# Performance work log

Measured on AMD Instinct MI355X. Metric: run time of the kernel, lower is better.

The kernel has to match this reference:

```python
import jax, jax.numpy as jnp
import numpy as np
import math

DIM = 1024
SEQ = 4096
BATCH = 4
CHUNK = 64
LN_EPS = 1e-5


def setup_inputs() -> dict:
    key = jax.random.key(0)
    ks = jax.random.split(key, 16)
    d = DIM
    def lin(k):
        k1, k2 = jax.random.split(k)
        lim = 1.0 / math.sqrt(d)
        W = jax.random.uniform(k1, (d, d), jnp.float32, -lim, lim)
        b = jax.random.uniform(k2, (d,), jnp.float32, -lim, lim)
        return W, b
    Wk, bk = lin(ks[0])
    Wv, bv = lin(ks[1])
    Wq, bq = lin(ks[2])
    Wkm, bkm = lin(ks[3])
    Wqm, bqm = lin(ks[4])
    Wo, bo = lin(ks[5])
    return {
        "x": jax.random.normal(ks[6], (BATCH, SEQ, d), jnp.float32),
        "base_phases": jax.random.normal(ks[7], (SEQ, d), jnp.float32) * math.pi,
        "Wk": Wk, "bk": bk, "Wv": Wv, "bv": bv, "Wq": Wq, "bq": bq,
        "Wkm": Wkm, "bkm": bkm, "Wqm": Wqm, "bqm": bqm,
        "mod_scale": jnp.ones((1,), jnp.float32) * 0.1,
        "ln_g": jnp.ones((d,), jnp.float32),
        "ln_b": jnp.zeros((d,), jnp.float32),
        "Wo": Wo, "bo": bo,
    }


def reference(x, base_phases, Wk, bk, Wv, bv, Wq, bq, Wkm, bkm, Wqm, bqm,
              mod_scale, ln_g, ln_b, Wo, bo):
    B, S, D = x.shape
    key = x @ Wk + bk
    value = x @ Wv + bv
    query = x @ Wq + bq
    base = base_phases[:S][None]                      # [1,S,D]
    key_phase = base + (key @ Wkm + bkm) * mod_scale   # [B,S,D]
    query_phase = base + (query @ Wqm + bqm) * mod_scale
    bound_real = value * jnp.cos(key_phase)
    bound_imag = value * jnp.sin(key_phase)
    pad = (CHUNK - S % CHUNK) % CHUNK
    if pad > 0:
        pcfg = ((0, 0), (0, pad), (0, 0))
        bound_real = jnp.pad(bound_real, pcfg)
        bound_imag = jnp.pad(bound_imag, pcfg)
        query_phase = jnp.pad(query_phase, pcfg)
    P = S + pad
    nc = P // CHUNK
    br = bound_real.reshape(B, nc, CHUNK, D)
    bi = bound_imag.reshape(B, nc, CHUNK, D)
    qp = query_phase.reshape(B, nc, CHUNK, D)
    mem_real = jnp.cumsum(br, axis=2)
    mem_imag = jnp.cumsum(bi, axis=2)
    retrieved = mem_real * jnp.cos(qp) + mem_imag * jnp.sin(qp)
    retrieved = retrieved.reshape(B, P, D)[:, :S] / math.sqrt(D)
    mu = jnp.mean(retrieved, axis=-1, keepdims=True)
    var = jnp.mean(jnp.square(retrieved - mu), axis=-1, keepdims=True)
    normed = (retrieved - mu) * jax.lax.rsqrt(var + LN_EPS) * ln_g + ln_b
    out = normed @ Wo + bo
    return x + out
```

## Files before the change

### kernel.cpp

```cpp
#include <hip/hip_runtime.h>

#define DIM 1024
#define SEQ 4096
#define MROWS 16384
#define CHUNK 64
#define NCHUNKBLKS 256

typedef float  f32x4  __attribute__((ext_vector_type(4)));
typedef __bf16 bf16x8 __attribute__((ext_vector_type(8)));
typedef __bf16 bf16x4 __attribute__((ext_vector_type(4)));

__device__ __forceinline__ void gld16(const void* g, void* l) {
  __builtin_amdgcn_global_load_lds((__attribute__((address_space(1))) void*)g,
                                   (__attribute__((address_space(3))) void*)l,
                                   16, 0, 0);
}

__device__ __forceinline__ f32x4 ld4f(const __bf16* p) {
  bf16x4 v = *(const bf16x4*)p;
  f32x4 r;
#pragma unroll
  for (int j = 0; j < 4; ++j) r[j] = (float)v[j];
  return r;
}

#define KLOOP64(As_, Bs_, Ag_, Bg_, AsL_, BsL_)                                  \
  for (int kt = 0; kt < DIM / 64; ++kt) {                                        \
    const __bf16* a_ = Ag_ + kt * 64;                                            \
    const __bf16* b_ = Bg_ + kt * 64;                                            \
    _Pragma("unroll") for (int i = 0; i < 4; ++i) {                              \
      gld16(a_ + i * 32 * DIM, AsL_ + i * 4096);                                 \
      gld16(b_ + i * 32 * DIM, BsL_ + i * 4096);                                 \
    }                                                                            \
    __syncthreads();                                                             \
    const bf16x8* Av_ = (const bf16x8*)(As_);                                    \
    const bf16x8* Bv_ = (const bf16x8*)(Bs_);                                    \
    _Pragma("unroll") for (int kk = 0; kk < 2; ++kk) {                           \
      bf16x8 af[4], bfv[4];                                                      \
      const int pc = (kk * 4 + kg) ^ (lane & 7);                                 \
      _Pragma("unroll") for (int i = 0; i < 4; ++i) af[i]  = Av_[(ar + i*16)*8 + pc]; \
      _Pragma("unroll") for (int i = 0; i < 4; ++i) bfv[i] = Bv_[(br + i*16)*8 + pc]; \
      _Pragma("unroll") for (int mi = 0; mi < 4; ++mi)                           \
        _Pragma("unroll") for (int ni = 0; ni < 4; ++ni)                         \
          acc[mi][ni] = __builtin_amdgcn_mfma_f32_16x16x32_bf16(af[mi], bfv[ni], acc[mi][ni], 0, 0, 0); \
    }                                                                            \
    __syncthreads();                                                             \
  }

#define GEMM_PROLOG64(A_, B_)                                                    \
  const int tid  = threadIdx.x;                                                  \
  const int lane = tid & 63;                                                     \
  const int widx = tid >> 6;                                                     \
  const int wr   = widx >> 1, wc = widx & 1;                                     \
  const int kc = ((lane & 7) ^ ((lane >> 3) & 7)) * 8;                           \
  const __bf16* Ag = (A_) + (size_t)(row0 + widx * 8 + (lane >> 3)) * DIM + kc;  \
  const __bf16* Bg = (B_) + (size_t)(col0 + widx * 8 + (lane >> 3)) * DIM + kc;  \
  char* AsL = (char*)As + widx * 1024;                                           \
  char* BsL = (char*)Bs + widx * 1024;                                           \
  f32x4 acc[4][4] = {};                                                          \
  const int ar = wr * 64 + (lane & 15);                                          \
  const int br = wc * 64 + (lane & 15);                                          \
  const int kg = lane >> 4;

template <int MODE, int SWZ>
__global__ __launch_bounds__(256, 2)
void gemm_bt(const __bf16* __restrict__ A, const __bf16* __restrict__ Bt,
             const float* __restrict__ bias, void* __restrict__ outp,
             const float* __restrict__ mscp, const float* __restrict__ xres,
             const __bf16* __restrict__ A2, const __bf16* __restrict__ Bt2,
             void* __restrict__ out2)
{
  __shared__ __bf16 As[128 * 64];
  __shared__ __bf16 Bs[128 * 64];
  if (MODE == 5 && blockIdx.z == 1) { A = A2; Bt = Bt2; outp = out2; }

  int row_t, col_t;
  if (SWZ == 1) {
    const int b = blockIdx.y * 8 + blockIdx.x;
    const int xcd = b & 7, slot = b >> 3;
    col_t = slot & 7;
    row_t = (xcd << 4) | (slot >> 3);
  } else {
    row_t = blockIdx.y; col_t = blockIdx.x;
  }
  const int row0 = row_t * 128, col0 = col_t * 128;

  GEMM_PROLOG64(A, Bt)
  KLOOP64(As, Bs, Ag, Bg, AsL, BsL)

  const int ccol = col0 + wc * 64 + (lane & 15);
  const int crow = row0 + wr * 64 + kg * 4;
  float bvv[4];
  if (MODE != 5) {
#pragma unroll
    for (int ni = 0; ni < 4; ++ni) bvv[ni] = bias[ccol + ni * 16];
  }
  float ms = 0.f;
  if (MODE == 5) ms = mscp[0];
#pragma unroll
  for (int mi = 0; mi < 4; ++mi)
#pragma unroll
    for (int ni = 0; ni < 4; ++ni)
#pragma unroll
      for (int r = 0; r < 4; ++r) {
        const int row = crow + mi * 16 + r;
        const int col = ccol + ni * 16;
        const size_t idx = (size_t)row * DIM + col;
        if (MODE == 3) {
          ((float*)outp)[idx] = acc[mi][ni][r] + bvv[ni] + xres[idx];
        } else {
          ((__bf16*)outp)[idx] = (__bf16)(acc[mi][ni][r] * ms);
        }
      }
}

__global__ __launch_bounds__(256, 2)
void gemm3(const __bf16* __restrict__ A, const __bf16* __restrict__ Ball,
           const float* __restrict__ biasAll,
           __bf16* __restrict__ valb, __bf16* __restrict__ kphb,
           __bf16* __restrict__ qphb)
{
  __shared__ __bf16 As[128 * 64];
  __shared__ __bf16 Bs[128 * 64];
  const int b = blockIdx.y * 24 + blockIdx.x;
  const int xcd = b & 7, p = b >> 3;
  const int col_t = p / 16;
  const int row_t = (xcd << 4) + (p & 15);
  const int row0 = row_t * 128, col0 = col_t * 128;

  GEMM_PROLOG64(A, Ball)
  KLOOP64(As, Bs, Ag, Bg, AsL, BsL)

  const int band = col_t >> 3;
  const int ccol = col0 + wc * 64 + (lane & 15);
  const int lcol0 = ccol & 1023;
  const int crow = row0 + wr * 64 + kg * 4;
  float bvv[4];
#pragma unroll
  for (int ni = 0; ni < 4; ++ni) bvv[ni] = biasAll[ccol + ni * 16];
  __bf16* outb = (band == 0) ? valb : (band == 1) ? kphb : qphb;
#pragma unroll
  for (int mi = 0; mi < 4; ++mi)
#pragma unroll
    for (int ni = 0; ni < 4; ++ni)
#pragma unroll
      for (int r = 0; r < 4; ++r) {
        const int row = crow + mi * 16 + r;
        const size_t idx = (size_t)row * DIM + lcol0 + ni * 16;
        outb[idx] = (__bf16)(acc[mi][ni][r] + bvv[ni]);
      }
}

__global__ __launch_bounds__(256)
void phasor_ln(const __bf16* __restrict__ val, const __bf16* __restrict__ kph,
               const __bf16* __restrict__ qph, const __bf16* __restrict__ baseb,
               const float* __restrict__ g, const float* __restrict__ lb,
               __bf16* __restrict__ nb)
{
  const int t = threadIdx.x;
  const int w = t >> 6, lane = t & 63;
  const size_t r0 = (size_t)blockIdx.x * CHUNK;
  const int c = t * 4;
  const f32x4 gv  = ((const f32x4*)g)[t];
  const f32x4 lbv = ((const f32x4*)lb)[t];
  __shared__ float redS[8][4], redQ[8][4];
  float mr[4] = {0.f, 0.f, 0.f, 0.f};
  float mi[4] = {0.f, 0.f, 0.f, 0.f};
  for (int rb = 0; rb < 8; ++rb) {
    float ret[8][4], ss[8], qq[8];
#pragma unroll
    for (int r = 0; r < 8; ++r) {
      const int row = rb * 8 + r;
      const size_t base = (r0 + row) * DIM + c;
      const f32x4 v  = ld4f(val + base);
      const f32x4 kp = ld4f(kph + base);
      const f32x4 qp = ld4f(qph + base);
      const f32x4 bp = ld4f(baseb + (size_t)((r0 + row) & (SEQ - 1)) * DIM + c);
      float s = 0.f, q = 0.f;
#pragma unroll
      for (int j = 0; j < 4; ++j) {
        float sk, ck, sq, cq;
        __sincosf(bp[j] + kp[j], &sk, &ck);
        mr[j] += v[j] * ck;
        mi[j] += v[j] * sk;
        __sincosf(bp[j] + qp[j], &sq, &cq);
        ret[r][j] = (mr[j] * cq + mi[j] * sq) * 0.03125f;
        s += ret[r][j];
        q += ret[r][j] * ret[r][j];
      }
      ss[r] = s; qq[r] = q;
    }
#pragma unroll
    for (int off = 32; off > 0; off >>= 1)
#pragma unroll
      for (int r = 0; r < 8; ++r) {
        ss[r] += __shfl_down(ss[r], off);
        qq[r] += __shfl_down(qq[r], off);
      }
    if (lane == 0)
#pragma unroll
      for (int r = 0; r < 8; ++r) { redS[r][w] = ss[r]; redQ[r][w] = qq[r]; }
    __syncthreads();
#pragma unroll
    for (int r = 0; r < 8; ++r) {
      const float mu   = (redS[r][0] + redS[r][1] + redS[r][2] + redS[r][3]) * (1.0f / DIM);
      const float varr = (redQ[r][0] + redQ[r][1] + redQ[r][2] + redQ[r][3]) * (1.0f / DIM) - mu * mu;
      const float rinv = rsqrtf(varr + 1e-5f);
      bf16x4 o;
#pragma unroll
      for (int j = 0; j < 4; ++j) o[j] = (__bf16)((ret[r][j] - mu) * rinv * gv[j] + lbv[j]);
      *(bf16x4*)(nb + (r0 + rb * 8 + r) * DIM + c) = o;
    }
    __syncthreads();
  }
}

__global__ void f2b_kernel(const float* __restrict__ in, __bf16* __restrict__ out, int n4) {
  int i = blockIdx.x * 256 + threadIdx.x;
  if (i >= n4) return;
  f32x4 vv = ((const f32x4*)in)[i];
  bf16x4 o;
#pragma unroll
  for (int j = 0; j < 4; ++j) o[j] = (__bf16)vv[j];
  ((bf16x4*)out)[i] = o;
}

__global__ void wrapb_kernel(const float* __restrict__ in, __bf16* __restrict__ out, int n4) {
  int i = blockIdx.x * 256 + threadIdx.x;
  if (i >= n4) return;
  f32x4 vv = ((const f32x4*)in)[i];
  bf16x4 o;
#pragma unroll
  for (int j = 0; j < 4; ++j) {
    float v = vv[j];
    v -= 6.2831853f * rintf(v * 0.15915494f);
    o[j] = (__bf16)v;
  }
  ((bf16x4*)out)[i] = o;
}

__global__ void f2b2_kernel(const float* __restrict__ i0, __bf16* __restrict__ o0,
                            const float* __restrict__ i1, __bf16* __restrict__ o1, int n4) {
  int i = blockIdx.x * 256 + threadIdx.x;
  if (i >= n4) return;
  const float* in = blockIdx.y ? i1 : i0;
  __bf16* out = blockIdx.y ? o1 : o0;
  f32x4 vv = ((const f32x4*)in)[i];
  bf16x4 o;
#pragma unroll
  for (int j = 0; j < 4; ++j) o[j] = (__bf16)vv[j];
  ((bf16x4*)out)[i] = o;
}

__global__ void transpose_f2b4(const float* __restrict__ s0, __bf16* __restrict__ d0,
                               const float* __restrict__ s1, __bf16* __restrict__ d1,
                               const float* __restrict__ s2, __bf16* __restrict__ d2,
                               const float* __restrict__ s3, __bf16* __restrict__ d3) {
  __shared__ float tle[32][33];
  const float* W; __bf16* Wt;
  switch (blockIdx.z) {
    case 0: W = s0; Wt = d0; break;
    case 1: W = s1; Wt = d1; break;
    case 2: W = s2; Wt = d2; break;
    default: W = s3; Wt = d3; break;
  }
  const int tx = threadIdx.x, ty = threadIdx.y;
  const int bx = blockIdx.x * 32, by = blockIdx.y * 32;
  for (int i = ty; i < 32; i += 8) tle[i][tx] = W[(size_t)(by + i) * DIM + bx + tx];
  __syncthreads();
  for (int i = ty; i < 32; i += 8) Wt[(size_t)(bx + i) * DIM + by + tx] = (__bf16)tle[tx][i];
}

__global__ void biasinit(const float* __restrict__ bv, const float* __restrict__ bkm,
                         const float* __restrict__ bqm, const float* __restrict__ ms,
                         float* __restrict__ biasAll) {
  const int n = blockIdx.x * 256 + threadIdx.x;
  const float m = ms[0];
  biasAll[n] = bv[n];
  biasAll[1024 + n] = bkm[n] * m;
  biasAll[2048 + n] = bqm[n] * m;
}

__global__ void biasacc(const float* __restrict__ bk, const float* __restrict__ Wkm,
                        const float* __restrict__ bq, const float* __restrict__ Wqm,
                        const float* __restrict__ ms, float* __restrict__ biasAll) {
  const int t = threadIdx.x;
  const int which = blockIdx.y;
  const int k0 = blockIdx.z * 128;
  const float* bs = which ? bq : bk;
  const float* W  = which ? Wqm : Wkm;
  const int n0 = t * 4;
  float s0 = 0.f, s1 = 0.f, s2 = 0.f, s3 = 0.f;
  for (int k = k0; k < k0 + 128; ++k) {
    const float b = bs[k];
    const f32x4 wv = *(const f32x4*)(W + (size_t)k * DIM + n0);
    s0 += b * wv[0]; s1 += b * wv[1]; s2 += b * wv[2]; s3 += b * wv[3];
  }
  const float m = ms[0];
  float* dst = biasAll + 1024 + which * 1024 + n0;
  atomicAdd(dst + 0, s0 * m);
  atomicAdd(dst + 1, s1 * m);
  atomicAdd(dst + 2, s2 * m);
  atomicAdd(dst + 3, s3 * m);
}

__global__ void copyx_kernel(const float* __restrict__ x, float* __restrict__ out, int n4) {
  int i = blockIdx.x * 256 + threadIdx.x;
  if (i >= n4) return;
  ((f32x4*)out)[i] = ((const f32x4*)x)[i];
}

extern "C" void kernel_launch(void* const* d_in, const int* in_sizes, int n_in,
                              void* d_out, int out_size, void* d_ws, size_t ws_size,
                              hipStream_t stream)
{
  (void)in_sizes; (void)n_in; (void)out_size;
  const float* x     = (const float*)d_in[0];
  const float* basep = (const float*)d_in[1];
  const float* Wk    = (const float*)d_in[2];
  const float* bk    = (const float*)d_in[3];
  const float* Wv    = (const float*)d_in[4];
  const float* bv    = (const float*)d_in[5];
  const float* Wq    = (const float*)d_in[6];
  const float* bq    = (const float*)d_in[7];
  const float* Wkm   = (const float*)d_in[8];
  const float* bkm   = (const float*)d_in[9];
  const float* Wqm   = (const float*)d_in[10];
  const float* bqm   = (const float*)d_in[11];
  const float* msc   = (const float*)d_in[12];
  const float* lng   = (const float*)d_in[13];
  const float* lnb   = (const float*)d_in[14];
  const float* Wo    = (const float*)d_in[15];
  const float* bo    = (const float*)d_in[16];

  char* ws = (char*)d_ws;
  const size_t MB = 1ull << 20;
  if (ws_size < 153 * MB) {
    copyx_kernel<<<MROWS * DIM / 4 / 256, 256, 0, stream>>>(x, (float*)d_out, MROWS * DIM / 4);
    return;
  }

  __bf16* xb     = (__bf16*)ws;
  __bf16* valb   = (__bf16*)(ws +  32 * MB);
  __bf16* kphb   = (__bf16*)(ws +  64 * MB);
  __bf16* qphb   = (__bf16*)(ws +  96 * MB);
  __bf16* Ball   = (__bf16*)(ws + 128 * MB);
  __bf16* WoT    = (__bf16*)(ws + 134 * MB);
  __bf16* TWkm   = (__bf16*)(ws + 136 * MB);
  __bf16* BWk    = (__bf16*)(ws + 138 * MB);
  __bf16* TWqm   = (__bf16*)(ws + 140 * MB);
  __bf16* BWq    = (__bf16*)(ws + 142 * MB);
  __bf16* baseb  = (__bf16*)(ws + 144 * MB);
  float*  biasAll= (float*)(ws + 152 * MB);
  __bf16* nbuf   = xb;

  f2b_kernel<<<MROWS * DIM / 4 / 256, 256, 0, stream>>>(x, xb, MROWS * DIM / 4);
  wrapb_kernel<<<SEQ * DIM / 4 / 256, 256, 0, stream>>>(basep, baseb, SEQ * DIM / 4);
  dim3 tg(32, 32, 4), tb(32, 8);
  transpose_f2b4<<<tg, tb, 0, stream>>>(Wv, Ball, Wo, WoT, Wkm, TWkm, Wqm, TWqm);
  f2b2_kernel<<<dim3(DIM * DIM / 4 / 256, 2), 256, 0, stream>>>(Wk, BWk, Wq, BWq, DIM * DIM / 4);
  gemm_bt<5, 0><<<dim3(8, 8, 2), 256, 0, stream>>>(
      TWkm, BWk, nullptr, Ball + (size_t)1024 * DIM, msc, nullptr,
      TWqm, BWq, Ball + (size_t)2048 * DIM);
  biasinit<<<4, 256, 0, stream>>>(bv, bkm, bqm, msc, biasAll);
  biasacc<<<dim3(1, 2, 8), 256, 0, stream>>>(bk, Wkm, bq, Wqm, msc, biasAll);

  gemm3<<<dim3(24, 128), 256, 0, stream>>>(xb, Ball, biasAll, valb, kphb, qphb);
  phasor_ln<<<NCHUNKBLKS, 256, 0, stream>>>(valb, kphb, qphb, baseb, lng, lnb, nbuf);
  gemm_bt<3, 1><<<dim3(8, 128), 256, 0, stream>>>(
      nbuf, WoT, bo, d_out, nullptr, x, nullptr, nullptr, nullptr);
}
```

Baseline: 264.9 us.

## Use 256x256 double-buffered MFMA GEMM tiles for main projections

Replaces the 128x128 single-buffered GEMMs for the fused V/K/Q projection and the output projection with a new 512-thread kernel using 256x256 tiles, double-buffered LDS staging via global_load_lds, and s_setprio around the MFMA bursts. Larger tiles raise arithmetic intensity per LDS load and cut global traffic, and prefetching the next K slice removes one barrier per iteration so loads overlap with compute. The cost is 128KB of LDS per block and many more accumulator registers, which may limit occupancy to one block per CU. The number of blocks also drops (256 for the output GEMM), which may leave CUs underused.

Measured after the change: 273.0 us. 1.03x slower.

```diff
diff --git a/kernel.cpp b/kernel.cpp
--- a/kernel.cpp
+++ b/kernel.cpp
@@ -22,6 +22,105 @@
 #pragma unroll
   for (int j = 0; j < 4; ++j) r[j] = (float)v[j];
   return r;
+}
+
+template <int MODE, int NCOLT>
+__global__ __launch_bounds__(512, 2)
+void gemm256(const __bf16* __restrict__ A, const __bf16* __restrict__ Bt,
+             const float* __restrict__ bias,
+             __bf16* __restrict__ ob0, __bf16* __restrict__ ob1,
+             __bf16* __restrict__ ob2,
+             float* __restrict__ of, const float* __restrict__ xres)
+{
+  __shared__ __bf16 As[2][256 * 64];
+  __shared__ __bf16 Bs[2][256 * 64];
+  const int tid  = threadIdx.x;
+  const int lane = tid & 63;
+  const int widx = tid >> 6;
+  const int wr = widx >> 2, wc = widx & 3;
+  const int bx  = blockIdx.x;
+  const int xcd = bx & 7, p = bx >> 3;
+  const int row_t = (xcd << 3) + (p & 7);
+  const int col_t = p >> 3;
+  const int row0 = row_t * 256, col0 = col_t * 256;
+
+  const int srow   = widx * 8 + (lane >> 3);
+  const int schunk = (lane & 7) ^ ((lane >> 3) & 7);
+  const __bf16* Ag = A  + (size_t)(row0 + srow) * DIM + schunk * 8;
+  const __bf16* Bg = Bt + (size_t)(col0 + srow) * DIM + schunk * 8;
+
+  f32x4 acc[8][4] = {};
+  const int arb = wr * 128 + (lane & 15);
+  const int brb = wc * 64  + (lane & 15);
+  const int kg = lane >> 4;
+  const int lx = lane & 7;
+
+#define STG(kt_, bu_) { \
+    const __bf16* a_ = Ag + (kt_) * 64; \
+    const __bf16* b_ = Bg + (kt_) * 64; \
+    char* ab_ = (char*)(&As[bu_][0]) + widx * 1024; \
+    char* bb_ = (char*)(&Bs[bu_][0]) + widx * 1024; \
+    _Pragma("unroll") for (int i_ = 0; i_ < 4; ++i_) { \
+      gld16(a_ + i_ * 64 * DIM, ab_ + i_ * 8192); \
+      gld16(b_ + i_ * 64 * DIM, bb_ + i_ * 8192); } }
+
+  STG(0, 0)
+  __syncthreads();
+  for (int kt = 0; kt < 16; ++kt) {
+    if (kt + 1 < 16) STG(kt + 1, (kt + 1) & 1)
+    __builtin_amdgcn_sched_barrier(0);
+    const bf16x8* Av = (const bf16x8*)(&As[kt & 1][0]);
+    const bf16x8* Bv = (const bf16x8*)(&Bs[kt & 1][0]);
+#pragma unroll
+    for (int kk = 0; kk < 2; ++kk) {
+      const int pc = (kk * 4 + kg) ^ lx;
+      bf16x8 af[8], bf[4];
+#pragma unroll
+      for (int i = 0; i < 8; ++i) af[i] = Av[(arb + i * 16) * 8 + pc];
+#pragma unroll
+      for (int i = 0; i < 4; ++i) bf[i] = Bv[(brb + i * 16) * 8 + pc];
+      __builtin_amdgcn_s_setprio(1);
+#pragma unroll
+      for (int mi = 0; mi < 8; ++mi)
+#pragma unroll
+        for (int ni = 0; ni < 4; ++ni)
+          acc[mi][ni] = __builtin_amdgcn_mfma_f32_16x16x32_bf16(af[mi], bf[ni], acc[mi][ni], 0, 0, 0);
+      __builtin_amdgcn_s_setprio(0);
+    }
+    __syncthreads();
+  }
+#undef STG
+
+  const int ccol  = col0 + wc * 64 + (lane & 15);
+  const int crow0 = row0 + wr * 128 + kg * 4;
+  float bvv[4];
+#pragma unroll
+  for (int ni = 0; ni < 4; ++ni) bvv[ni] = bias[ccol + ni * 16];
+  if (MODE == 0) {
+    const int band = col_t >> 2;
+    const int lcol0 = ccol & 1023;
+    __bf16* outb = (band == 0) ? ob0 : (band == 1) ? ob1 : ob2;
+#pragma unroll
+    for (int mi = 0; mi < 8; ++mi)
+#pragma unroll
+      for (int ni = 0; ni < 4; ++ni)
+#pragma unroll
+        for (int r = 0; r < 4; ++r) {
+          const int row = crow0 + mi * 16 + r;
+          outb[(size_t)row * DIM + lcol0 + ni * 16] = (__bf16)(acc[mi][ni][r] + bvv[ni]);
+        }
+  } else {
+#pragma unroll
+    for (int mi = 0; mi < 8; ++mi)
+#pragma unroll
+      for (int ni = 0; ni < 4; ++ni)
+#pragma unroll
+        for (int r = 0; r < 4; ++r) {
+          const int row = crow0 + mi * 16 + r;
+          const size_t idx = (size_t)row * DIM + ccol + ni * 16;
+          of[idx] = acc[mi][ni][r] + bvv[ni] + xres[idx];
+        }
+  }
 }
 
 #define KLOOP64(As_, Bs_, Ag_, Bg_, AsL_, BsL_)                                  \
@@ -47,56 +146,35 @@
     __syncthreads();                                                             \
   }
 
-#define GEMM_PROLOG64(A_, B_)                                                    \
-  const int tid  = threadIdx.x;                                                  \
-  const int lane = tid & 63;                                                     \
-  const int widx = tid >> 6;                                                     \
-  const int wr   = widx >> 1, wc = widx & 1;                                     \
-  const int kc = ((lane & 7) ^ ((lane >> 3) & 7)) * 8;                           \
-  const __bf16* Ag = (A_) + (size_t)(row0 + widx * 8 + (lane >> 3)) * DIM + kc;  \
-  const __bf16* Bg = (B_) + (size_t)(col0 + widx * 8 + (lane >> 3)) * DIM + kc;  \
-  char* AsL = (char*)As + widx * 1024;                                           \
-  char* BsL = (char*)Bs + widx * 1024;                                           \
-  f32x4 acc[4][4] = {};                                                          \
-  const int ar = wr * 64 + (lane & 15);                                          \
-  const int br = wc * 64 + (lane & 15);                                          \
-  const int kg = lane >> 4;
-
-template <int MODE, int SWZ>
 __global__ __launch_bounds__(256, 2)
-void gemm_bt(const __bf16* __restrict__ A, const __bf16* __restrict__ Bt,
-             const float* __restrict__ bias, void* __restrict__ outp,
-             const float* __restrict__ mscp, const float* __restrict__ xres,
+void gemm_wc(const __bf16* __restrict__ A, const __bf16* __restrict__ Bt,
+             void* __restrict__ outp, const float* __restrict__ mscp,
              const __bf16* __restrict__ A2, const __bf16* __restrict__ Bt2,
              void* __restrict__ out2)
 {
   __shared__ __bf16 As[128 * 64];
   __shared__ __bf16 Bs[128 * 64];
-  if (MODE == 5 && blockIdx.z == 1) { A = A2; Bt = Bt2; outp = out2; }
-
-  int row_t, col_t;
-  if (SWZ == 1) {
-    const int b = blockIdx.y * 8 + blockIdx.x;
-    const int xcd = b & 7, slot = b >> 3;
-    col_t = slot & 7;
-    row_t = (xcd << 4) | (slot >> 3);
-  } else {
-    row_t = blockIdx.y; col_t = blockIdx.x;
-  }
-  const int row0 = row_t * 128, col0 = col_t * 128;
-
-  GEMM_PROLOG64(A, Bt)
+  if (blockIdx.z == 1) { A = A2; Bt = Bt2; outp = out2; }
+  const int row0 = blockIdx.y * 128, col0 = blockIdx.x * 128;
+  const int tid  = threadIdx.x;
+  const int lane = tid & 63;
+  const int widx = tid >> 6;
+  const int wr   = widx >> 1, wc = widx & 1;
+  const int kc = ((lane & 7) ^ ((lane >> 3) & 7)) * 8;
+  const __bf16* Ag = A  + (size_t)(row0 + widx * 8 + (lane >> 3)) * DIM + kc;
+  const __bf16* Bg = Bt + (size_t)(col0 + widx * 8 + (lane >> 3)) * DIM + kc;
+  char* AsL = (char*)As + widx * 1024;
+  char* BsL = (char*)Bs + widx * 1024;
+  f32x4 acc[4][4] = {};
+  const int ar = wr * 64 + (lane & 15);
+  const int br = wc * 64 + (lane & 15);
+  const int kg = lane >> 4;
+
   KLOOP64(As, Bs, Ag, Bg, AsL, BsL)
 
   const int ccol = col0 + wc * 64 + (lane & 15);
   const int crow = row0 + wr * 64 + kg * 4;
-  float bvv[4];
-  if (MODE != 5) {
-#pragma unroll
-    for (int ni = 0; ni < 4; ++ni) bvv[ni] = bias[ccol + ni * 16];
-  }
-  float ms = 0.f;
-  if (MODE == 5) ms = mscp[0];
+  const float ms = mscp[0];
 #pragma unroll
   for (int mi = 0; mi < 4; ++mi)
 #pragma unroll
@@ -105,49 +183,7 @@
       for (int r = 0; r < 4; ++r) {
         const int row = crow + mi * 16 + r;
         const int col = ccol + ni * 16;
-        const size_t idx = (size_t)row * DIM + col;
-        if (MODE == 3) {
-          ((float*)outp)[idx] = acc[mi][ni][r] + bvv[ni] + xres[idx];
-        } else {
-          ((__bf16*)outp)[idx] = (__bf16)(acc[mi][ni][r] * ms);
-        }
-      }
-}
-
-__global__ __launch_bounds__(256, 2)
-void gemm3(const __bf16* __restrict__ A, const __bf16* __restrict__ Ball,
-           const float* __restrict__ biasAll,
-           __bf16* __restrict__ valb, __bf16* __restrict__ kphb,
-           __bf16* __restrict__ qphb)
-{
-  __shared__ __bf16 As[128 * 64];
-  __shared__ __bf16 Bs[128 * 64];
-  const int b = blockIdx.y * 24 + blockIdx.x;
-  const int xcd = b & 7, p = b >> 3;
-  const int col_t = p / 16;
-  const int row_t = (xcd << 4) + (p & 15);
-  const int row0 = row_t * 128, col0 = col_t * 128;
-
-  GEMM_PROLOG64(A, Ball)
-  KLOOP64(As, Bs, Ag, Bg, AsL, BsL)
-
-  const int band = col_t >> 3;
-  const int ccol = col0 + wc * 64 + (lane & 15);
-  const int lcol0 = ccol & 1023;
-  const int crow = row0 + wr * 64 + kg * 4;
-  float bvv[4];
-#pragma unroll
-  for (int ni = 0; ni < 4; ++ni) bvv[ni] = biasAll[ccol + ni * 16];
-  __bf16* outb = (band == 0) ? valb : (band == 1) ? kphb : qphb;
-#pragma unroll
-  for (int mi = 0; mi < 4; ++mi)
-#pragma unroll
-    for (int ni = 0; ni < 4; ++ni)
-#pragma unroll
-      for (int r = 0; r < 4; ++r) {
-        const int row = crow + mi * 16 + r;
-        const size_t idx = (size_t)row * DIM + lcol0 + ni * 16;
-        outb[idx] = (__bf16)(acc[mi][ni][r] + bvv[ni]);
+        ((__bf16*)outp)[(size_t)row * DIM + col] = (__bf16)(acc[mi][ni][r] * ms);
       }
 }
 
@@ -359,14 +395,15 @@
   dim3 tg(32, 32, 4), tb(32, 8);
   transpose_f2b4<<<tg, tb, 0, stream>>>(Wv, Ball, Wo, WoT, Wkm, TWkm, Wqm, TWqm);
   f2b2_kernel<<<dim3(DIM * DIM / 4 / 256, 2), 256, 0, stream>>>(Wk, BWk, Wq, BWq, DIM * DIM / 4);
-  gemm_bt<5, 0><<<dim3(8, 8, 2), 256, 0, stream>>>(
-      TWkm, BWk, nullptr, Ball + (size_t)1024 * DIM, msc, nullptr,
+  gemm_wc<<<dim3(8, 8, 2), 256, 0, stream>>>(
+      TWkm, BWk, Ball + (size_t)1024 * DIM, msc,
       TWqm, BWq, Ball + (size_t)2048 * DIM);
   biasinit<<<4, 256, 0, stream>>>(bv, bkm, bqm, msc, biasAll);
   biasacc<<<dim3(1, 2, 8), 256, 0, stream>>>(bk, Wkm, bq, Wqm, msc, biasAll);
 
-  gemm3<<<dim3(24, 128), 256, 0, stream>>>(xb, Ball, biasAll, valb, kphb, qphb);
+  gemm256<0, 12><<<768, 512, 0, stream>>>(xb, Ball, biasAll,
+                                          valb, kphb, qphb, nullptr, nullptr);
   phasor_ln<<<NCHUNKBLKS, 256, 0, stream>>>(valb, kphb, qphb, baseb, lng, lnb, nbuf);
-  gemm_bt<3, 1><<<dim3(8, 128), 256, 0, stream>>>(
-      nbuf, WoT, bo, d_out, nullptr, x, nullptr, nullptr, nullptr);
-}
+  gemm256<1, 4><<<256, 512, 0, stream>>>(nbuf, WoT, bo,
+                                         nullptr, nullptr, nullptr, (float*)d_out, x);
+}
```

## Merge prep kernels and read bf16 residual in final GEMM

Applied to the files above, without the earlier changes.

Merges the x cast, phase wrap and bias init into one launch, and folds the Wk/Wq casts into the weight transpose launch, cutting kernel launches. The final GEMM now reads the residual from the bf16 copy of x instead of fp32 x, halving residual read traffic. To keep xb alive it writes the layernorm output into the kph buffer in place, so phasor_ln drops restrict on those pointers. The residual loses precision because it is now added from bf16.

After: 248.9 us. -6.0%, faster.

```diff
diff --git a/kernel.cpp b/kernel.cpp
--- a/kernel.cpp
+++ b/kernel.cpp
@@ -62,27 +62,17 @@
   const int br = wc * 64 + (lane & 15);                                          \
   const int kg = lane >> 4;
 
-template <int MODE, int SWZ>
 __global__ __launch_bounds__(256, 2)
-void gemm_bt(const __bf16* __restrict__ A, const __bf16* __restrict__ Bt,
-             const float* __restrict__ bias, void* __restrict__ outp,
-             const float* __restrict__ mscp, const float* __restrict__ xres,
-             const __bf16* __restrict__ A2, const __bf16* __restrict__ Bt2,
-             void* __restrict__ out2)
+void gemm_fin(const __bf16* __restrict__ A, const __bf16* __restrict__ Bt,
+              const float* __restrict__ bias, float* __restrict__ of,
+              const __bf16* __restrict__ xres)
 {
   __shared__ __bf16 As[128 * 64];
   __shared__ __bf16 Bs[128 * 64];
-  if (MODE == 5 && blockIdx.z == 1) { A = A2; Bt = Bt2; outp = out2; }
-
-  int row_t, col_t;
-  if (SWZ == 1) {
-    const int b = blockIdx.y * 8 + blockIdx.x;
-    const int xcd = b & 7, slot = b >> 3;
-    col_t = slot & 7;
-    row_t = (xcd << 4) | (slot >> 3);
-  } else {
-    row_t = blockIdx.y; col_t = blockIdx.x;
-  }
+  const int b = blockIdx.y * 8 + blockIdx.x;
+  const int xcd = b & 7, slot = b >> 3;
+  const int col_t = slot & 7;
+  const int row_t = (xcd << 4) | (slot >> 3);
   const int row0 = row_t * 128, col0 = col_t * 128;
 
   GEMM_PROLOG64(A, Bt)
@@ -91,12 +81,37 @@
   const int ccol = col0 + wc * 64 + (lane & 15);
   const int crow = row0 + wr * 64 + kg * 4;
   float bvv[4];
-  if (MODE != 5) {
-#pragma unroll
-    for (int ni = 0; ni < 4; ++ni) bvv[ni] = bias[ccol + ni * 16];
-  }
-  float ms = 0.f;
-  if (MODE == 5) ms = mscp[0];
+#pragma unroll
+  for (int ni = 0; ni < 4; ++ni) bvv[ni] = bias[ccol + ni * 16];
+#pragma unroll
+  for (int mi = 0; mi < 4; ++mi)
+#pragma unroll
+    for (int ni = 0; ni < 4; ++ni)
+#pragma unroll
+      for (int r = 0; r < 4; ++r) {
+        const int row = crow + mi * 16 + r;
+        const size_t idx = (size_t)row * DIM + ccol + ni * 16;
+        of[idx] = acc[mi][ni][r] + bvv[ni] + (float)xres[idx];
+      }
+}
+
+__global__ __launch_bounds__(256, 2)
+void gemm_wc(const __bf16* __restrict__ A, const __bf16* __restrict__ Bt,
+             void* __restrict__ outp, const float* __restrict__ mscp,
+             const __bf16* __restrict__ A2, const __bf16* __restrict__ Bt2,
+             void* __restrict__ out2)
+{
+  __shared__ __bf16 As[128 * 64];
+  __shared__ __bf16 Bs[128 * 64];
+  if (blockIdx.z == 1) { A = A2; Bt = Bt2; outp = out2; }
+  const int row0 = blockIdx.y * 128, col0 = blockIdx.x * 128;
+
+  GEMM_PROLOG64(A, Bt)
+  KLOOP64(As, Bs, Ag, Bg, AsL, BsL)
+
+  const int ccol = col0 + wc * 64 + (lane & 15);
+  const int crow = row0 + wr * 64 + kg * 4;
+  const float ms = mscp[0];
 #pragma unroll
   for (int mi = 0; mi < 4; ++mi)
 #pragma unroll
@@ -105,12 +120,7 @@
       for (int r = 0; r < 4; ++r) {
         const int row = crow + mi * 16 + r;
         const int col = ccol + ni * 16;
-        const size_t idx = (size_t)row * DIM + col;
-        if (MODE == 3) {
-          ((float*)outp)[idx] = acc[mi][ni][r] + bvv[ni] + xres[idx];
-        } else {
-          ((__bf16*)outp)[idx] = (__bf16)(acc[mi][ni][r] * ms);
-        }
+        ((__bf16*)outp)[(size_t)row * DIM + col] = (__bf16)(acc[mi][ni][r] * ms);
       }
 }
 
@@ -152,10 +162,10 @@
 }
 
 __global__ __launch_bounds__(256)
-void phasor_ln(const __bf16* __restrict__ val, const __bf16* __restrict__ kph,
+void phasor_ln(const __bf16* __restrict__ val, const __bf16* kph,
                const __bf16* __restrict__ qph, const __bf16* __restrict__ baseb,
                const float* __restrict__ g, const float* __restrict__ lb,
-               __bf16* __restrict__ nb)
+               __bf16* nb)
 {
   const int t = threadIdx.x;
   const int w = t >> 6, lane = t & 63;
@@ -215,70 +225,69 @@
   }
 }
 
-__global__ void f2b_kernel(const float* __restrict__ in, __bf16* __restrict__ out, int n4) {
-  int i = blockIdx.x * 256 + threadIdx.x;
-  if (i >= n4) return;
-  f32x4 vv = ((const f32x4*)in)[i];
-  bf16x4 o;
-#pragma unroll
-  for (int j = 0; j < 4; ++j) o[j] = (__bf16)vv[j];
-  ((bf16x4*)out)[i] = o;
-}
-
-__global__ void wrapb_kernel(const float* __restrict__ in, __bf16* __restrict__ out, int n4) {
-  int i = blockIdx.x * 256 + threadIdx.x;
-  if (i >= n4) return;
-  f32x4 vv = ((const f32x4*)in)[i];
-  bf16x4 o;
-#pragma unroll
-  for (int j = 0; j < 4; ++j) {
-    float v = vv[j];
-    v -= 6.2831853f * rintf(v * 0.15915494f);
-    o[j] = (__bf16)v;
-  }
-  ((bf16x4*)out)[i] = o;
-}
-
-__global__ void f2b2_kernel(const float* __restrict__ i0, __bf16* __restrict__ o0,
-                            const float* __restrict__ i1, __bf16* __restrict__ o1, int n4) {
-  int i = blockIdx.x * 256 + threadIdx.x;
-  if (i >= n4) return;
-  const float* in = blockIdx.y ? i1 : i0;
-  __bf16* out = blockIdx.y ? o1 : o0;
-  f32x4 vv = ((const f32x4*)in)[i];
-  bf16x4 o;
-#pragma unroll
-  for (int j = 0; j < 4; ++j) o[j] = (__bf16)vv[j];
-  ((bf16x4*)out)[i] = o;
-}
-
-__global__ void transpose_f2b4(const float* __restrict__ s0, __bf16* __restrict__ d0,
-                               const float* __restrict__ s1, __bf16* __restrict__ d1,
-                               const float* __restrict__ s2, __bf16* __restrict__ d2,
-                               const float* __restrict__ s3, __bf16* __restrict__ d3) {
+#define NB_F2B   (MROWS * DIM / 4 / 256)
+#define NB_WRAP  (SEQ * DIM / 4 / 256)
+__global__ void prep_misc(const float* __restrict__ x, __bf16* __restrict__ xb,
+                          const float* __restrict__ basep, __bf16* __restrict__ baseb,
+                          const float* __restrict__ bv, const float* __restrict__ bkm,
+                          const float* __restrict__ bqm, const float* __restrict__ ms,
+                          float* __restrict__ biasAll)
+{
+  const int blk = blockIdx.x;
+  if (blk < NB_F2B) {
+    const int i = blk * 256 + threadIdx.x;
+    f32x4 vv = ((const f32x4*)x)[i];
+    bf16x4 o;
+#pragma unroll
+    for (int j = 0; j < 4; ++j) o[j] = (__bf16)vv[j];
+    ((bf16x4*)xb)[i] = o;
+  } else if (blk < NB_F2B + NB_WRAP) {
+    const int i = (blk - NB_F2B) * 256 + threadIdx.x;
+    f32x4 vv = ((const f32x4*)basep)[i];
+    bf16x4 o;
+#pragma unroll
+    for (int j = 0; j < 4; ++j) {
+      float v = vv[j];
+      v -= 6.2831853f * rintf(v * 0.15915494f);
+      o[j] = (__bf16)v;
+    }
+    ((bf16x4*)baseb)[i] = o;
+  } else {
+    const int n = (blk - NB_F2B - NB_WRAP) * 256 + threadIdx.x;
+    const float m = ms[0];
+    biasAll[n] = bv[n];
+    biasAll[1024 + n] = bkm[n] * m;
+    biasAll[2048 + n] = bqm[n] * m;
+  }
+}
+
+__global__ void wprep6(const float* __restrict__ s0, __bf16* __restrict__ d0,
+                       const float* __restrict__ s1, __bf16* __restrict__ d1,
+                       const float* __restrict__ s2, __bf16* __restrict__ d2,
+                       const float* __restrict__ s3, __bf16* __restrict__ d3,
+                       const float* __restrict__ s4, __bf16* __restrict__ d4,
+                       const float* __restrict__ s5, __bf16* __restrict__ d5)
+{
   __shared__ float tle[32][33];
   const float* W; __bf16* Wt;
   switch (blockIdx.z) {
     case 0: W = s0; Wt = d0; break;
     case 1: W = s1; Wt = d1; break;
     case 2: W = s2; Wt = d2; break;
-    default: W = s3; Wt = d3; break;
+    case 3: W = s3; Wt = d3; break;
+    case 4: W = s4; Wt = d4; break;
+    default: W = s5; Wt = d5; break;
   }
   const int tx = threadIdx.x, ty = threadIdx.y;
   const int bx = blockIdx.x * 32, by = blockIdx.y * 32;
-  for (int i = ty; i < 32; i += 8) tle[i][tx] = W[(size_t)(by + i) * DIM + bx + tx];
-  __syncthreads();
-  for (int i = ty; i < 32; i += 8) Wt[(size_t)(bx + i) * DIM + by + tx] = (__bf16)tle[tx][i];
-}
-
-__global__ void biasinit(const float* __restrict__ bv, const float* __restrict__ bkm,
-                         const float* __restrict__ bqm, const float* __restrict__ ms,
-                         float* __restrict__ biasAll) {
-  const int n = blockIdx.x * 256 + threadIdx.x;
-  const float m = ms[0];
-  biasAll[n] = bv[n];
-  biasAll[1024 + n] = bkm[n] * m;
-  biasAll[2048 + n] = bqm[n] * m;
+  if (blockIdx.z < 4) {
+    for (int i = ty; i < 32; i += 8) tle[i][tx] = W[(size_t)(by + i) * DIM + bx + tx];
+    __syncthreads();
+    for (int i = ty; i < 32; i += 8) Wt[(size_t)(bx + i) * DIM + by + tx] = (__bf16)tle[tx][i];
+  } else {
+    for (int i = ty; i < 32; i += 8)
+      Wt[(size_t)(by + i) * DIM + bx + tx] = (__bf16)W[(size_t)(by + i) * DIM + bx + tx];
+  }
 }
 
 __global__ void biasacc(const float* __restrict__ bk, const float* __restrict__ Wkm,
@@ -352,21 +361,18 @@
   __bf16* BWq    = (__bf16*)(ws + 142 * MB);
   __bf16* baseb  = (__bf16*)(ws + 144 * MB);
   float*  biasAll= (float*)(ws + 152 * MB);
-  __bf16* nbuf   = xb;
-
-  f2b_kernel<<<MROWS * DIM / 4 / 256, 256, 0, stream>>>(x, xb, MROWS * DIM / 4);
-  wrapb_kernel<<<SEQ * DIM / 4 / 256, 256, 0, stream>>>(basep, baseb, SEQ * DIM / 4);
-  dim3 tg(32, 32, 4), tb(32, 8);
-  transpose_f2b4<<<tg, tb, 0, stream>>>(Wv, Ball, Wo, WoT, Wkm, TWkm, Wqm, TWqm);
-  f2b2_kernel<<<dim3(DIM * DIM / 4 / 256, 2), 256, 0, stream>>>(Wk, BWk, Wq, BWq, DIM * DIM / 4);
-  gemm_bt<5, 0><<<dim3(8, 8, 2), 256, 0, stream>>>(
-      TWkm, BWk, nullptr, Ball + (size_t)1024 * DIM, msc, nullptr,
+  __bf16* nbuf   = kphb;
+
+  prep_misc<<<NB_F2B + NB_WRAP + 4, 256, 0, stream>>>(x, xb, basep, baseb,
+                                                      bv, bkm, bqm, msc, biasAll);
+  wprep6<<<dim3(32, 32, 6), dim3(32, 8), 0, stream>>>(
+      Wv, Ball, Wo, WoT, Wkm, TWkm, Wqm, TWqm, Wk, BWk, Wq, BWq);
+  gemm_wc<<<dim3(8, 8, 2), 256, 0, stream>>>(
+      TWkm, BWk, Ball + (size_t)1024 * DIM, msc,
       TWqm, BWq, Ball + (size_t)2048 * DIM);
-  biasinit<<<4, 256, 0, stream>>>(bv, bkm, bqm, msc, biasAll);
   biasacc<<<dim3(1, 2, 8), 256, 0, stream>>>(bk, Wkm, bq, Wqm, msc, biasAll);
 
   gemm3<<<dim3(24, 128), 256, 0, stream>>>(xb, Ball, biasAll, valb, kphb, qphb);
   phasor_ln<<<NCHUNKBLKS, 256, 0, stream>>>(valb, kphb, qphb, baseb, lng, lnb, nbuf);
-  gemm_bt<3, 1><<<dim3(8, 128), 256, 0, stream>>>(
-      nbuf, WoT, bo, d_out, nullptr, x, nullptr, nullptr, nullptr);
-}
+  gemm_fin<<<dim3(8, 128), 256, 0, stream>>>(nbuf, WoT, bo, (float*)d_out, xb);
+}
```
